# Kernel optimization log

Hardware: AMD Instinct MI355X
Metric: run time of the kernel (lower is better)

Reference implementation:

```python
import jax, jax.numpy as jnp
import numpy as np

C = 64
C8 = C // 8
C16 = C // 16


def setup_inputs() -> dict:
    key = jax.random.key(0)
    ks = jax.random.split(key, 11)
    s = lambda fan_in: 1.0 / np.sqrt(fan_in)
    return {
        "x": jax.random.normal(ks[0], (4, C, 64, 64), dtype=jnp.float32),
        # 1x1 convs == per-pixel linear: weight [out, in], bias [out]
        "Wq": jax.random.uniform(ks[1], (C8, C), minval=-s(C), maxval=s(C)),
        "bq": jax.random.uniform(ks[2], (C8,), minval=-s(C), maxval=s(C)),
        "Wk": jax.random.uniform(ks[3], (C8, C), minval=-s(C), maxval=s(C)),
        "bk": jax.random.uniform(ks[4], (C8,), minval=-s(C), maxval=s(C)),
        "Wv": jax.random.uniform(ks[5], (C, C), minval=-s(C), maxval=s(C)),
        "bv": jax.random.uniform(ks[6], (C,), minval=-s(C), maxval=s(C)),
        "W1": jax.random.uniform(ks[7], (C16, C), minval=-s(C), maxval=s(C)),
        "b1": jax.random.uniform(ks[8], (C16,), minval=-s(C), maxval=s(C)),
        "W2": jax.random.uniform(ks[9], (C, C16), minval=-s(C16), maxval=s(C16)),
        "b2": jax.random.uniform(ks[10], (C,), minval=-s(C16), maxval=s(C16)),
    }


def reference(x, Wq, bq, Wk, bk, Wv, bv, W1, b1, W2, b2):
    b, c, h, w = x.shape
    n = h * w
    xf = x.reshape(b, c, n)                                   # [b,c,n]
    Q = jnp.einsum('qc,bcn->bnq', Wq, xf) + bq                # [b,n,c/8]
    K = jnp.einsum('kc,bcn->bkn', Wk, xf) + bk[None, :, None] # [b,c/8,n]
    V = jnp.einsum('vc,bcn->bvn', Wv, xf) + bv[None, :, None] # [b,c,n]
    scores = jnp.einsum('bnq,bqm->bnm', Q, K) / jnp.sqrt(jnp.float32(c))
    att = jax.nn.softmax(scores, axis=-1)                     # [b,n,n]
    # self_attention_map = V @ att^T
    sa = jnp.einsum('bvm,bnm->bvn', V, att).reshape(b, c, h, w)
    # SE-style channel gate
    avg = xf.mean(axis=2)                                     # [b,c]
    gate = jax.nn.sigmoid(jax.nn.relu(avg @ W1.T + b1) @ W2.T + b2)
    return sa * gate[:, :, None, None]
```

## Files before the change

### kernel.cpp

```cpp
#include <hip/hip_runtime.h>
#include <hip/hip_bf16.h>

typedef __attribute__((ext_vector_type(8))) short bf16x8;
typedef __attribute__((ext_vector_type(4))) float f32x4;
typedef __attribute__((ext_vector_type(4))) unsigned short u16x4;
typedef __attribute__((ext_vector_type(8))) unsigned short u16x8;

#define WS_QB 0
#define WS_KB 131072
#define WS_VB 262144
#define WS_AVG_U 1310720

__device__ __forceinline__ unsigned short bf_hi(float x) {
    __hip_bfloat16 h = __float2bfloat16(x);
    return *reinterpret_cast<unsigned short*>(&h);
}

__global__ __launch_bounds__(256) void proj_kernel(
    const float* __restrict__ x,
    const float* __restrict__ Wq, const float* __restrict__ bq,
    const float* __restrict__ Wk, const float* __restrict__ bk,
    const float* __restrict__ Wv, const float* __restrict__ bv,
    unsigned short* __restrict__ Qb, unsigned short* __restrict__ Kb,
    unsigned short* __restrict__ Vb, float* __restrict__ avg)
{
    __shared__ __align__(16) unsigned short Wls[16 * 72];

    const int tid = threadIdx.x;
    const int w = tid >> 6;
    const int l = tid & 63;
    const int g = l >> 4;
    const int l15 = l & 15;

    const int tile = blockIdx.x >> 8;
    const int pair = blockIdx.x & 255;
    const int b = pair >> 6;
    const int n0 = (pair & 63) << 6;
    const int n = n0 + w * 16 + l15;
    const float* xb = x + b * 262144;

    float xr[2][8];
#pragma unroll
    for (int kcb = 0; kcb < 2; ++kcb)
#pragma unroll
        for (int j = 0; j < 8; ++j)
            xr[kcb][j] = xb[(kcb * 32 + g * 8 + j) * 4096 + n];

#pragma unroll
    for (int i = 0; i < 4; ++i) {
        const int idx = i * 256 + tid;
        const int row = idx >> 6, col = idx & 63;
        float wv;
        if (tile == 0) wv = (row < 8) ? Wq[row * 64 + col] : Wk[(row - 8) * 64 + col];
        else           wv = Wv[((tile - 1) * 16 + row) * 64 + col];
        Wls[row * 72 + col] = bf_hi(wv);
    }
    __syncthreads();

    bf16x8 bfr[2];
#pragma unroll
    for (int kcb = 0; kcb < 2; ++kcb)
#pragma unroll
        for (int j = 0; j < 8; ++j)
            bfr[kcb][j] = (short)bf_hi(xr[kcb][j]);

    const bf16x8 a0 = *(const bf16x8*)&Wls[l15 * 72 + g * 8];
    const bf16x8 a1 = *(const bf16x8*)&Wls[l15 * 72 + 32 + g * 8];
    f32x4 acc;
#pragma unroll
    for (int r = 0; r < 4; ++r) acc[r] = 0.0f;
    acc = __builtin_amdgcn_mfma_f32_16x16x32_bf16(a0, bfr[0], acc, 0, 0, 0);
    acc = __builtin_amdgcn_mfma_f32_16x16x32_bf16(a1, bfr[1], acc, 0, 0, 0);

    if (tile == 0) {
        u16x4 ov;
        if (g < 2) {
#pragma unroll
            for (int r = 0; r < 4; ++r) ov[r] = bf_hi((acc[r] + bq[g * 4 + r]) * 0.125f);
            *(u16x4*)&Qb[(b * 4096 + n) * 8 + g * 4] = ov;
        } else {
#pragma unroll
            for (int r = 0; r < 4; ++r) ov[r] = bf_hi(acc[r] + bk[(g - 2) * 4 + r]);
            *(u16x4*)&Kb[(b * 4096 + n) * 8 + (g - 2) * 4] = ov;
        }
        const int c = tid >> 2;
        const float* xrow = xb + c * 4096 + n0 + ((tid & 3) << 4);
        float s = 0.0f;
#pragma unroll
        for (int k = 0; k < 4; ++k) {
            const float4 v = *(const float4*)&xrow[k * 4];
            s += (v.x + v.y) + (v.z + v.w);
        }
        s += __shfl_xor(s, 1);
        s += __shfl_xor(s, 2);
        if ((tid & 3) == 0) atomicAdd(&avg[b * 64 + c], s * (1.0f / 4096.0f));
    } else {
#pragma unroll
        for (int r = 0; r < 4; ++r) {
            const int v = (tile - 1) * 16 + g * 4 + r;
            Vb[(b * 64 + v) * 4096 + n] = bf_hi(acc[r] + bv[v]);
        }
    }
}

__global__ __launch_bounds__(256, 2) void attn_kernel(
    const unsigned short* __restrict__ Qb, const unsigned short* __restrict__ Kb,
    const unsigned short* __restrict__ Vb, const float* __restrict__ avg,
    const float* __restrict__ W1, const float* __restrict__ b1,
    const float* __restrict__ W2, const float* __restrict__ b2,
    float* __restrict__ out)
{
    __shared__ __align__(16) unsigned short Pls[4][2][32][40];
    __shared__ float osum[4][64][33];
    __shared__ float zls[32], gls[64], avgs[64];

    const int t = threadIdx.x;
    const int w = t >> 6;
    const int l = t & 63;
    const int g = l >> 4;
    const int l15 = l & 15;

    const int wg = (blockIdx.x & 7) * 64 + (blockIdx.x >> 3);
    const int b = wg >> 7;
    const int q0 = (wg & 127) << 5;

    if (t < 32) zls[t] = 0.0f;
    if (t < 64) avgs[t] = avg[b * 64 + t];
    __syncthreads();

    bf16x8 zf = {};
    bf16x8 qf[2];
#pragma unroll
    for (int qt = 0; qt < 2; ++qt) {
        bf16x8 v = *(const bf16x8*)&Qb[(b * 4096 + q0 + qt * 16 + l15) * 8];
        qf[qt] = (g == 0) ? v : zf;
    }

    const unsigned short* kb = Kb + b * 4096 * 8;
    const unsigned short* vbB = Vb + (b * 64) * 4096;

    int m0 = w * 32;
    bf16x8 kpa = zf, kpb = zf;
    if (g == 0) {
        kpa = *(const bf16x8*)&kb[(m0 + l15) * 8];
        kpb = *(const bf16x8*)&kb[(m0 + 16 + l15) * 8];
    }
    bf16x8 vp[4];
#pragma unroll
    for (int vt = 0; vt < 4; ++vt)
        vp[vt] = *(const bf16x8*)&vbB[(vt * 16 + l15) * 4096 + m0 + g * 8];

    f32x4 acc[2][4];
#pragma unroll
    for (int qt = 0; qt < 2; ++qt)
#pragma unroll
        for (int vt = 0; vt < 4; ++vt)
#pragma unroll
            for (int r = 0; r < 4; ++r) acc[qt][vt][r] = 0.0f;
    float zreg[2] = {0.f, 0.f};

    for (int ci = 0; ci < 32; ++ci) {
        const bf16x8 ka = kpa, kc = kpb;
        bf16x8 vc[4];
#pragma unroll
        for (int vt = 0; vt < 4; ++vt) vc[vt] = vp[vt];

        const int m0n = (ci < 31) ? (w + 4 * (ci + 1)) * 32 : m0;
        if (g == 0) {
            kpa = *(const bf16x8*)&kb[(m0n + l15) * 8];
            kpb = *(const bf16x8*)&kb[(m0n + 16 + l15) * 8];
        }
#pragma unroll
        for (int vt = 0; vt < 4; ++vt)
            vp[vt] = *(const bf16x8*)&vbB[(vt * 16 + l15) * 4096 + m0n + g * 8];

        unsigned short* Pw = &Pls[w][ci & 1][0][0];
        f32x4 dz;
#pragma unroll
        for (int r = 0; r < 4; ++r) dz[r] = 0.0f;
#pragma unroll
        for (int mt = 0; mt < 2; ++mt) {
            const bf16x8 kf = mt ? kc : ka;
#pragma unroll
            for (int qt = 0; qt < 2; ++qt) {
                f32x4 d = __builtin_amdgcn_mfma_f32_16x16x32_bf16(kf, qf[qt], dz, 0, 0, 0);
                float p[4];
#pragma unroll
                for (int r = 0; r < 4; ++r) p[r] = __expf(d[r]);
                zreg[qt] += (p[0] + p[1]) + (p[2] + p[3]);
                u16x4 pw;
#pragma unroll
                for (int r = 0; r < 4; ++r) pw[r] = bf_hi(p[r]);
                *(u16x4*)&Pw[(qt * 16 + l15) * 40 + mt * 16 + g * 4] = pw;
            }
        }
        const bf16x8 bp0 = *(const bf16x8*)&Pw[l15 * 40 + g * 8];
        const bf16x8 bp1 = *(const bf16x8*)&Pw[(16 + l15) * 40 + g * 8];

        __builtin_amdgcn_s_setprio(1);
#pragma unroll
        for (int vt = 0; vt < 4; ++vt) {
            acc[0][vt] = __builtin_amdgcn_mfma_f32_16x16x32_bf16(vc[vt], bp0, acc[0][vt], 0, 0, 0);
            acc[1][vt] = __builtin_amdgcn_mfma_f32_16x16x32_bf16(vc[vt], bp1, acc[1][vt], 0, 0, 0);
        }
        __builtin_amdgcn_s_setprio(0);
        m0 = m0n;
    }

#pragma unroll
    for (int qt = 0; qt < 2; ++qt) {
        float z = zreg[qt];
        z += __shfl_xor(z, 16);
        z += __shfl_xor(z, 32);
        if (g == 0) atomicAdd(&zls[qt * 16 + l15], z);
    }

#pragma unroll
    for (int qt = 0; qt < 2; ++qt)
#pragma unroll
        for (int vt = 0; vt < 4; ++vt)
#pragma unroll
            for (int r = 0; r < 4; ++r)
                osum[w][vt * 16 + g * 4 + r][qt * 16 + l15] = acc[qt][vt][r];

    if (t < 64) {
        float hreg[4];
#pragma unroll
        for (int j = 0; j < 4; ++j) {
            float hh = b1[j];
            for (int c = 0; c < 64; ++c) hh += W1[j * 64 + c] * avgs[c];
            hreg[j] = fmaxf(hh, 0.0f);
        }
        float gg = b2[t];
#pragma unroll
        for (int j = 0; j < 4; ++j) gg += W2[t * 4 + j] * hreg[j];
        gls[t] = 1.0f / (1.0f + __expf(-gg));
    }
    __syncthreads();

    {
        const int v = t >> 2;
        const int qb4 = (t & 3) * 8;
        const float gv = gls[v];
        float* orow = out + (b * 64 + v) * 4096 + q0 + qb4;
#pragma unroll
        for (int j = 0; j < 8; ++j) {
            const int q = qb4 + j;
            const float s = (osum[0][v][q] + osum[1][v][q])
                          + (osum[2][v][q] + osum[3][v][q]);
            orow[j] = s * (1.0f / zls[q]) * gv;
        }
    }
}

extern "C" void kernel_launch(void* const* d_in, const int* in_sizes, int n_in,
                              void* d_out, int out_size, void* d_ws, size_t ws_size,
                              hipStream_t stream) {
    const float* x  = (const float*)d_in[0];
    const float* Wq = (const float*)d_in[1];
    const float* bq = (const float*)d_in[2];
    const float* Wk = (const float*)d_in[3];
    const float* bk = (const float*)d_in[4];
    const float* Wv = (const float*)d_in[5];
    const float* bv = (const float*)d_in[6];
    const float* W1 = (const float*)d_in[7];
    const float* b1 = (const float*)d_in[8];
    const float* W2 = (const float*)d_in[9];
    const float* b2 = (const float*)d_in[10];

    unsigned short* wsu = (unsigned short*)d_ws;
    unsigned short* Qb = wsu + WS_QB;
    unsigned short* Kb = wsu + WS_KB;
    unsigned short* Vb = wsu + WS_VB;
    float* avg = (float*)(wsu + WS_AVG_U);
    float* out = (float*)d_out;

    hipMemsetAsync(avg, 0, 256 * sizeof(float), stream);
    proj_kernel<<<1280, 256, 0, stream>>>(x, Wq, bq, Wk, bk, Wv, bv, Qb, Kb, Vb, avg);
    attn_kernel<<<512, 256, 0, stream>>>(Qb, Kb, Vb, avg, W1, b1, W2, b2, out);
}
```

Measured before the change: 117.7 us.

## Pass attention probabilities between MFMAs in registers via lane shuffles instead of LDS

Drops the per-wave shared-memory staging buffer for the softmax probabilities P. The layout of the score MFMA output is now matched to the B-operand of the PV MFMA by packing bf16 pairs and exchanging half of them with a lane-xor-16 shuffle. The V loads are remapped with a permuted lane-group index so the k-dimension order stays consistent. This removes the LDS writes and reads from the inner loop and frees shared memory, and the launch bound is raised to 4 blocks per SM to allow more occupancy, at the cost of tighter register limits.

```diff
diff --git a/kernel.cpp b/kernel.cpp
--- a/kernel.cpp
+++ b/kernel.cpp
@@ -14,6 +14,9 @@
 __device__ __forceinline__ unsigned short bf_hi(float x) {
     __hip_bfloat16 h = __float2bfloat16(x);
     return *reinterpret_cast<unsigned short*>(&h);
+}
+__device__ __forceinline__ unsigned int bfpk(float lo, float hi) {
+    return (unsigned int)bf_hi(lo) | ((unsigned int)bf_hi(hi) << 16);
 }
 
 __global__ __launch_bounds__(256) void proj_kernel(
@@ -103,14 +106,13 @@
     }
 }
 
-__global__ __launch_bounds__(256, 2) void attn_kernel(
+__global__ __launch_bounds__(256, 4) void attn_kernel(
     const unsigned short* __restrict__ Qb, const unsigned short* __restrict__ Kb,
     const unsigned short* __restrict__ Vb, const float* __restrict__ avg,
     const float* __restrict__ W1, const float* __restrict__ b1,
     const float* __restrict__ W2, const float* __restrict__ b2,
     float* __restrict__ out)
 {
-    __shared__ __align__(16) unsigned short Pls[4][2][32][40];
     __shared__ float osum[4][64][33];
     __shared__ float zls[32], gls[64], avgs[64];
 
@@ -119,6 +121,8 @@
     const int l = t & 63;
     const int g = l >> 4;
     const int l15 = l & 15;
+    const int godd = g & 1;
+    const int gs = (godd << 1) | (g >> 1);
 
     const int wg = (blockIdx.x & 7) * 64 + (blockIdx.x >> 3);
     const int b = wg >> 7;
@@ -148,7 +152,7 @@
     bf16x8 vp[4];
 #pragma unroll
     for (int vt = 0; vt < 4; ++vt)
-        vp[vt] = *(const bf16x8*)&vbB[(vt * 16 + l15) * 4096 + m0 + g * 8];
+        vp[vt] = *(const bf16x8*)&vbB[(vt * 16 + l15) * 4096 + m0 + gs * 8];
 
     f32x4 acc[2][4];
 #pragma unroll
@@ -172,36 +176,41 @@
         }
 #pragma unroll
         for (int vt = 0; vt < 4; ++vt)
-            vp[vt] = *(const bf16x8*)&vbB[(vt * 16 + l15) * 4096 + m0n + g * 8];
-
-        unsigned short* Pw = &Pls[w][ci & 1][0][0];
+            vp[vt] = *(const bf16x8*)&vbB[(vt * 16 + l15) * 4096 + m0n + gs * 8];
+
         f32x4 dz;
 #pragma unroll
         for (int r = 0; r < 4; ++r) dz[r] = 0.0f;
-#pragma unroll
-        for (int mt = 0; mt < 2; ++mt) {
-            const bf16x8 kf = mt ? kc : ka;
-#pragma unroll
-            for (int qt = 0; qt < 2; ++qt) {
-                f32x4 d = __builtin_amdgcn_mfma_f32_16x16x32_bf16(kf, qf[qt], dz, 0, 0, 0);
-                float p[4];
-#pragma unroll
-                for (int r = 0; r < 4; ++r) p[r] = __expf(d[r]);
-                zreg[qt] += (p[0] + p[1]) + (p[2] + p[3]);
-                u16x4 pw;
-#pragma unroll
-                for (int r = 0; r < 4; ++r) pw[r] = bf_hi(p[r]);
-                *(u16x4*)&Pw[(qt * 16 + l15) * 40 + mt * 16 + g * 4] = pw;
-            }
-        }
-        const bf16x8 bp0 = *(const bf16x8*)&Pw[l15 * 40 + g * 8];
-        const bf16x8 bp1 = *(const bf16x8*)&Pw[(16 + l15) * 40 + g * 8];
+
+        bf16x8 bp[2];
+#pragma unroll
+        for (int qt = 0; qt < 2; ++qt) {
+            f32x4 d0 = __builtin_amdgcn_mfma_f32_16x16x32_bf16(ka, qf[qt], dz, 0, 0, 0);
+            f32x4 d1 = __builtin_amdgcn_mfma_f32_16x16x32_bf16(kc, qf[qt], dz, 0, 0, 0);
+            float p0[4], p1[4];
+#pragma unroll
+            for (int r = 0; r < 4; ++r) { p0[r] = __expf(d0[r]); p1[r] = __expf(d1[r]); }
+            zreg[qt] += ((p0[0] + p0[1]) + (p0[2] + p0[3]))
+                      + ((p1[0] + p1[1]) + (p1[2] + p1[3]));
+            const unsigned int A = bfpk(p0[0], p0[1]), B = bfpk(p0[2], p0[3]);
+            const unsigned int C = bfpk(p1[0], p1[1]), D = bfpk(p1[2], p1[3]);
+            const unsigned int s1 = godd ? A : C;
+            const unsigned int s2 = godd ? B : D;
+            const unsigned int r1 = __shfl_xor(s1, 16);
+            const unsigned int r2 = __shfl_xor(s2, 16);
+            union { unsigned int u[4]; bf16x8 v; } pw;
+            pw.u[0] = godd ? r1 : A;
+            pw.u[1] = godd ? r2 : B;
+            pw.u[2] = godd ? C : r1;
+            pw.u[3] = godd ? D : r2;
+            bp[qt] = pw.v;
+        }
 
         __builtin_amdgcn_s_setprio(1);
 #pragma unroll
         for (int vt = 0; vt < 4; ++vt) {
-            acc[0][vt] = __builtin_amdgcn_mfma_f32_16x16x32_bf16(vc[vt], bp0, acc[0][vt], 0, 0, 0);
-            acc[1][vt] = __builtin_amdgcn_mfma_f32_16x16x32_bf16(vc[vt], bp1, acc[1][vt], 0, 0, 0);
+            acc[0][vt] = __builtin_amdgcn_mfma_f32_16x16x32_bf16(vc[vt], bp[0], acc[0][vt], 0, 0, 0);
+            acc[1][vt] = __builtin_amdgcn_mfma_f32_16x16x32_bf16(vc[vt], bp[1], acc[1][vt], 0, 0, 0);
         }
         __builtin_amdgcn_s_setprio(0);
         m0 = m0n;
```

Measured after the change: 117.6 us. Within noise of the previous version (-0.1%).
